# Kernel tuning notes

Measured on AMD Instinct MI355X. Metric: run time of the kernel, lower is better.

## Reference

```python
import jax, jax.numpy as jnp
import numpy as np

B, S, DIM = 2, 2048, 2048
H, KVH, D = 16, 8, 128
EPS = 1e-6
ROPE_BASE = 1000000.0
MAX_SEQ = 8192


def _build_rope(max_seq, dim, base):
    inv_freq = 1.0 / (base ** (np.arange(0, dim, 2, dtype=np.float64) / dim))
    t = np.arange(max_seq, dtype=np.float64)
    freqs = np.outer(t, inv_freq)  # [max_seq, dim//2]
    return (jnp.asarray(np.cos(freqs), jnp.float32),
            jnp.asarray(np.sin(freqs), jnp.float32))


def setup_inputs() -> dict:
    key = jax.random.key(0)
    ks = jax.random.split(key, 7)
    scale = 0.02
    cos_cache, sin_cache = _build_rope(MAX_SEQ, D, ROPE_BASE)
    return {
        "x": jax.random.normal(ks[0], (B, S, DIM), jnp.float32),
        "wq": jax.random.normal(ks[1], (DIM, H * D), jnp.float32) * scale,
        "wk": jax.random.normal(ks[2], (DIM, KVH * D), jnp.float32) * scale,
        "wv": jax.random.normal(ks[3], (DIM, KVH * D), jnp.float32) * scale,
        "wo": jax.random.normal(ks[4], (H * D, DIM), jnp.float32) * scale,
        "q_gamma": 1.0 + 0.01 * jax.random.normal(ks[5], (D,), jnp.float32),
        "k_gamma": 1.0 + 0.01 * jax.random.normal(ks[6], (D,), jnp.float32),
        "cos_cache": cos_cache,
        "sin_cache": sin_cache,
    }


def _rmsnorm(t, gamma):
    var = jnp.mean(t * t, axis=-1, keepdims=True)
    return t * jax.lax.rsqrt(var + EPS) * gamma


def _rotate_half(t):
    t1, t2 = jnp.split(t, 2, axis=-1)
    return jnp.concatenate((-t2, t1), axis=-1)


def _apply_rope(t, cos, sin):
    # t: [B, S, heads, D]; cos/sin: [S, D//2]
    cos_f = jnp.concatenate((cos, cos), axis=-1)[None, :, None, :]
    sin_f = jnp.concatenate((sin, sin), axis=-1)[None, :, None, :]
    return t * cos_f + _rotate_half(t) * sin_f


def reference(x, wq, wk, wv, wo, q_gamma, k_gamma, cos_cache, sin_cache):
    b, s, _ = x.shape
    q = (x @ wq).reshape(b, s, H, D)
    k = (x @ wk).reshape(b, s, KVH, D)
    v = (x @ wv).reshape(b, s, KVH, D)
    q = _rmsnorm(q, q_gamma)
    k = _rmsnorm(k, k_gamma)
    # prefill: kv_len == q_len == s, cache empty
    cos, sin = cos_cache[:s], sin_cache[:s]
    q = _apply_rope(q, cos, sin)
    k = _apply_rope(k, cos, sin)
    # -> [B, heads, S, D]
    q = q.transpose(0, 2, 1, 3)
    k = k.transpose(0, 2, 1, 3)
    v = v.transpose(0, 2, 1, 3)
    # GQA: repeat_interleave kv heads
    g = H // KVH
    k = jnp.repeat(k, g, axis=1)
    v = jnp.repeat(v, g, axis=1)
    scale = 1.0 / jnp.sqrt(jnp.asarray(D, x.dtype))
    scores = jnp.einsum("bhqd,bhkd->bhqk", q, k) * scale
    causal = jnp.tril(jnp.ones((s, s), bool))
    scores = jnp.where(causal, scores, jnp.finfo(scores.dtype).min)
    attn = jax.nn.softmax(scores, axis=-1)
    out = jnp.einsum("bhqk,bhkd->bhqd", attn, v)
    out = out.transpose(0, 2, 1, 3).reshape(b, s, H * D)
    return out @ wo
```

## Files before the change

### kernel.cpp

```cpp
#include <hip/hip_runtime.h>
#include <hip/hip_bf16.h>


typedef __attribute__((ext_vector_type(8))) short s16x8;
typedef __attribute__((ext_vector_type(4))) float f32x4;

typedef const __attribute__((address_space(1))) void* gas_t;
typedef __attribute__((address_space(3))) void* las_t;
#define GLL16(g, l) __builtin_amdgcn_global_load_lds((gas_t)(const void*)(g), (las_t)(void*)(l), 16, 0, 0)

static __device__ __forceinline__ unsigned short f2bf(float f) {
    union { float f; unsigned u; } v; v.f = f;
    unsigned r = v.u + 0x7FFF + ((v.u >> 16) & 1);
    return (unsigned short)(r >> 16);
}
static __device__ __forceinline__ float bf2f(unsigned short h) {
    union { unsigned u; float f; } v; v.u = ((unsigned)h) << 16;
    return v.f;
}
static __device__ __forceinline__ float exp2_fast(float x) {
    float r; asm("v_exp_f32 %0, %1" : "=v"(r) : "v"(x)); return r;
}

#define SCALE_L2E 0.12751744900929f

__global__ __launch_bounds__(256) void k_convert_x(const float* __restrict__ x,
                                                   unsigned short* __restrict__ xb, int n) {
    int i = (blockIdx.x * 256 + threadIdx.x) * 8;
    if (i >= n) return;
    float4 a = *(const float4*)(x + i);
    float4 b = *(const float4*)(x + i + 4);
    s16x8 o;
    o[0] = (short)f2bf(a.x); o[1] = (short)f2bf(a.y); o[2] = (short)f2bf(a.z); o[3] = (short)f2bf(a.w);
    o[4] = (short)f2bf(b.x); o[5] = (short)f2bf(b.y); o[6] = (short)f2bf(b.z); o[7] = (short)f2bf(b.w);
    *(s16x8*)(xb + i) = o;
}

__global__ __launch_bounds__(256) void k_transpose_w(const float* __restrict__ src,
                                                     unsigned short* __restrict__ dst,
                                                     int K, int N, int nbase, int dstld) {
    __shared__ float t[32][33];
    int k0 = blockIdx.x * 32, n0 = blockIdx.y * 32;
    int tx = threadIdx.x & 31, ty0 = threadIdx.x >> 5;
    for (int p = 0; p < 4; p++) {
        int ty = ty0 + p * 8;
        t[ty][tx] = src[(size_t)(k0 + ty) * N + n0 + tx];
    }
    __syncthreads();
    for (int p = 0; p < 4; p++) {
        int ty = ty0 + p * 8;
        dst[(size_t)(nbase + n0 + ty) * dstld + k0 + tx] = f2bf(t[tx][ty]);
    }
}

__global__ __launch_bounds__(256) void k_transpose_v(const unsigned short* __restrict__ V,
                                                     unsigned short* __restrict__ Vt) {
    __shared__ unsigned short t[32][33];
    int s0 = blockIdx.x * 32, d0 = blockIdx.y * 32;
    size_t base = (size_t)blockIdx.z * 2048 * 128;
    int tx = threadIdx.x & 31, ty0 = threadIdx.x >> 5;
    for (int p = 0; p < 4; p++) {
        int ty = ty0 + p * 8;
        t[ty][tx] = V[base + (size_t)(s0 + ty) * 128 + d0 + tx];
    }
    __syncthreads();
    for (int p = 0; p < 4; p++) {
        int ty = ty0 + p * 8;
        Vt[base + (size_t)(d0 + ty) * 2048 + s0 + tx] = t[tx][ty];
    }
}

template<int OUTF32>
__global__ __launch_bounds__(512, 2) void k_gemm256(const unsigned short* __restrict__ A,
                                                    const unsigned short* __restrict__ Bt,
                                                    void* __restrict__ Cout,
                                                    int M, int N, int K) {
    __shared__ unsigned short As[2][256 * 64];
    __shared__ unsigned short Bs[2][256 * 64];
    int tid = threadIdx.x, lane = tid & 63, wave = tid >> 6;
    int wm = wave >> 2, wn = wave & 3;
    int lr = lane & 15, lg = lane >> 4;
    int srow = wave * 8 + (lane >> 3);
    int scol = (((lane & 7) ^ (lane >> 3)) * 8);
    const unsigned short* Ag = A  + (size_t)(blockIdx.x * 256 + srow) * K + scol;
    const unsigned short* Bg = Bt + (size_t)(blockIdx.y * 256 + srow) * K + scol;
    int ldsoff = wave * 512;

    f32x4 acc[8][4] = {};
    int NK = K / 64;
    #pragma unroll
    for (int p = 0; p < 4; p++) {
        GLL16(Ag + (size_t)p * 64 * K, &As[0][p * 4096 + ldsoff]);
        GLL16(Bg + (size_t)p * 64 * K, &Bs[0][p * 4096 + ldsoff]);
    }
    for (int t = 0; t < NK; ++t) {
        int slot = t & 1, nslot = slot ^ 1;
        size_t kn = (size_t)(t + 1) * 64;
        bool more = (t + 1) < NK;
        if (more) {
            GLL16(Ag + kn, &As[nslot][ldsoff]);
            GLL16(Bg + kn, &Bs[nslot][ldsoff]);
            asm volatile("s_waitcnt vmcnt(2)" ::: "memory");
        } else {
            asm volatile("s_waitcnt vmcnt(0)" ::: "memory");
        }
        __builtin_amdgcn_s_barrier();
        asm volatile("" ::: "memory");
        s16x8 bf[4][2];
        #pragma unroll
        for (int n = 0; n < 4; n++)
            #pragma unroll
            for (int kk = 0; kk < 2; kk++)
                bf[n][kk] = *(const s16x8*)&Bs[slot][(wn * 64 + n * 16 + lr) * 64 +
                                                     ((kk * 32 + lg * 8) ^ ((lr & 7) << 3))];
        #pragma unroll
        for (int q = 0; q < 4; q++) {
            s16x8 af[2][2];
            #pragma unroll
            for (int mm = 0; mm < 2; mm++)
                #pragma unroll
                for (int kk = 0; kk < 2; kk++)
                    af[mm][kk] = *(const s16x8*)&As[slot][(wm * 128 + (q * 2 + mm) * 16 + lr) * 64 +
                                                          ((kk * 32 + lg * 8) ^ ((lr & 7) << 3))];
            if (more && q < 3) {
                GLL16(Ag + (size_t)(q + 1) * 64 * K + kn, &As[nslot][(q + 1) * 4096 + ldsoff]);
                GLL16(Bg + (size_t)(q + 1) * 64 * K + kn, &Bs[nslot][(q + 1) * 4096 + ldsoff]);
            }
            __builtin_amdgcn_s_barrier();
            __builtin_amdgcn_s_setprio(1);
            #pragma unroll
            for (int mm = 0; mm < 2; mm++)
                #pragma unroll
                for (int n = 0; n < 4; n++)
                    #pragma unroll
                    for (int kk = 0; kk < 2; kk++)
                        acc[q * 2 + mm][n] = __builtin_amdgcn_mfma_f32_16x16x32_bf16(
                            af[mm][kk], bf[n][kk], acc[q * 2 + mm][n], 0, 0, 0);
            __builtin_amdgcn_s_setprio(0);
            __builtin_amdgcn_s_barrier();
        }
    }
    int rbase = blockIdx.x * 256 + wm * 128;
    int cbase = blockIdx.y * 256 + wn * 64;
    #pragma unroll
    for (int am = 0; am < 8; am++)
        #pragma unroll
        for (int n = 0; n < 4; n++)
            #pragma unroll
            for (int r = 0; r < 4; r++) {
                int row = rbase + am * 16 + lg * 4 + r;
                int col = cbase + n * 16 + lr;
                float v = acc[am][n][r];
                if (OUTF32) ((float*)Cout)[(size_t)row * N + col] = v;
                else        ((unsigned short*)Cout)[(size_t)row * N + col] = f2bf(v);
            }
}

template<int OUTF32>
__global__ __launch_bounds__(256) void k_gemm_bt(const unsigned short* __restrict__ A,
                                                 const unsigned short* __restrict__ Bt,
                                                 void* __restrict__ Cout,
                                                 int M, int N, int K) {
    __shared__ unsigned short As[128 * 32];
    __shared__ unsigned short Bs[128 * 32];
    int tid = threadIdx.x;
    int lane = tid & 63;
    int wave = tid >> 6;
    int wm = wave >> 1, wn = wave & 1;
    int lr = lane & 15, lk = (lane >> 4) * 8;
    int srow = wave * 32 + (lane >> 2);
    int scol = (lane & 3) * 8;
    const unsigned short* Ag0 = A  + (size_t)(blockIdx.x * 128 + srow) * K + scol;
    const unsigned short* Ag1 = Ag0 + (size_t)16 * K;
    const unsigned short* Bg0 = Bt + (size_t)(blockIdx.y * 128 + srow) * K + scol;
    const unsigned short* Bg1 = Bg0 + (size_t)16 * K;
    unsigned short* Asw = &As[wave * 1024];
    unsigned short* Bsw = &Bs[wave * 1024];
    f32x4 acc[4][4] = {};
    for (int k0 = 0; k0 < K; k0 += 32) {
        __syncthreads();
        GLL16(Ag0 + k0, Asw);
        GLL16(Ag1 + k0, Asw + 512);
        GLL16(Bg0 + k0, Bsw);
        GLL16(Bg1 + k0, Bsw + 512);
        __syncthreads();
        s16x8 af[4], bfr[4];
        #pragma unroll
        for (int m = 0; m < 4; m++) af[m]  = *(const s16x8*)&As[(wm * 64 + m * 16 + lr) * 32 + lk];
        #pragma unroll
        for (int n = 0; n < 4; n++) bfr[n] = *(const s16x8*)&Bs[(wn * 64 + n * 16 + lr) * 32 + lk];
        #pragma unroll
        for (int m = 0; m < 4; m++)
            #pragma unroll
            for (int n = 0; n < 4; n++)
                acc[m][n] = __builtin_amdgcn_mfma_f32_16x16x32_bf16(af[m], bfr[n], acc[m][n], 0, 0, 0);
    }
    int rbase = blockIdx.x * 128 + wm * 64;
    int cbase = blockIdx.y * 128 + wn * 64;
    #pragma unroll
    for (int m = 0; m < 4; m++)
        #pragma unroll
        for (int n = 0; n < 4; n++)
            #pragma unroll
            for (int r = 0; r < 4; r++) {
                int row = rbase + m * 16 + (lane >> 4) * 4 + r;
                int col = cbase + n * 16 + lr;
                float v = acc[m][n][r];
                if (OUTF32) ((float*)Cout)[(size_t)row * N + col] = v;
                else        ((unsigned short*)Cout)[(size_t)row * N + col] = f2bf(v);
            }
}

__global__ __launch_bounds__(256) void k_rms_rope(const unsigned short* __restrict__ qkv,
                                                  const float* __restrict__ qg,
                                                  const float* __restrict__ kg,
                                                  const float* __restrict__ cosc,
                                                  const float* __restrict__ sinc,
                                                  unsigned short* __restrict__ Qt,
                                                  unsigned short* __restrict__ Kt,
                                                  unsigned short* __restrict__ Vt) {
    int r = blockIdx.x;
    int b = r >> 11;
    int s = r & 2047;
    int tid = threadIdx.x;
    int wave = tid >> 6, lane = tid & 63;
    int sl = lane >> 4;
    int li = lane & 15;
    int d0 = li * 8;
    const unsigned short* row = qkv + (size_t)r * 4096;
    #pragma unroll
    for (int p = 0; p < 2; p++) {
        int seg = p * 16 + wave * 4 + sl;
        s16x8 raw = *(const s16x8*)(row + seg * 128 + d0);
        if (seg >= 24) {
            *(s16x8*)(Vt + ((size_t)(b * 8 + (seg - 24)) * 2048 + s) * 128 + d0) = raw;
            continue;
        }
        float e[8];
        #pragma unroll
        for (int j = 0; j < 8; j++) e[j] = bf2f((unsigned short)raw[j]);
        float ssq = 0.f;
        #pragma unroll
        for (int j = 0; j < 8; j++) ssq += e[j] * e[j];
        ssq += __shfl_xor(ssq, 1, 64);
        ssq += __shfl_xor(ssq, 2, 64);
        ssq += __shfl_xor(ssq, 4, 64);
        ssq += __shfl_xor(ssq, 8, 64);
        float rn = rsqrtf(ssq * (1.0f / 128.0f) + 1e-6f);
        const float* g = (seg < 16) ? qg : kg;
        float gs = (seg < 16) ? SCALE_L2E : 1.0f;
        float4 g0 = *(const float4*)(g + d0);
        float4 g1 = *(const float4*)(g + d0 + 4);
        float t[8];
        t[0] = e[0] * rn * g0.x * gs; t[1] = e[1] * rn * g0.y * gs;
        t[2] = e[2] * rn * g0.z * gs; t[3] = e[3] * rn * g0.w * gs;
        t[4] = e[4] * rn * g1.x * gs; t[5] = e[5] * rn * g1.y * gs;
        t[6] = e[6] * rn * g1.z * gs; t[7] = e[7] * rn * g1.w * gs;
        float pr[8];
        #pragma unroll
        for (int j = 0; j < 8; j++) pr[j] = __shfl_xor(t[j], 8, 64);
        int didx = d0 & 63;
        float4 c0 = *(const float4*)(cosc + (size_t)s * 64 + didx);
        float4 c1 = *(const float4*)(cosc + (size_t)s * 64 + didx + 4);
        float4 sn0 = *(const float4*)(sinc + (size_t)s * 64 + didx);
        float4 sn1 = *(const float4*)(sinc + (size_t)s * 64 + didx + 4);
        float cv[8] = {c0.x, c0.y, c0.z, c0.w, c1.x, c1.y, c1.z, c1.w};
        float sv[8] = {sn0.x, sn0.y, sn0.z, sn0.w, sn1.x, sn1.y, sn1.z, sn1.w};
        float sgn = (li < 8) ? -1.0f : 1.0f;
        s16x8 o;
        #pragma unroll
        for (int j = 0; j < 8; j++)
            o[j] = (short)f2bf(t[j] * cv[j] + sgn * pr[j] * sv[j]);
        unsigned short* dst = (seg < 16)
            ? Qt + ((size_t)(b * 16 + seg) * 2048 + s) * 128 + d0
            : Kt + ((size_t)(b * 8 + (seg - 16)) * 2048 + s) * 128 + d0;
        *(s16x8*)dst = o;
    }
}

__global__ __launch_bounds__(512, 4) void k_attn(const unsigned short* __restrict__ Qt,
                                                 const unsigned short* __restrict__ Kt,
                                                 const unsigned short* __restrict__ Vtg,
                                                 unsigned short* __restrict__ attn) {
    __shared__ unsigned short Ks[64][136];
    __shared__ unsigned short Vs[128][72];
    __shared__ unsigned short Ps[8][16][72];
    int bid = blockIdx.x;
    int lo = bid & 255;
    int qb, bh;
    if (bid < 256) { qb = lo & 15;        bh = lo >> 4; }
    else           { qb = 15 - (lo & 15); bh = 16 + (lo >> 4); }
    int b = bh >> 4, h = bh & 15;
    int kvh = h >> 1;
    int tid = threadIdx.x;
    int lane = tid & 63, wave = tid >> 6;
    int lr = lane & 15, lg = lane >> 4;
    int q0 = qb * 128;
    const unsigned short* Qb1 = Qt + ((size_t)bh * 2048 + q0 + wave * 16) * 128;
    const unsigned short* Kbase = Kt + (size_t)(b * 8 + kvh) * 2048 * 128;
    const unsigned short* Vtb   = Vtg + (size_t)(b * 8 + kvh) * 128 * 2048;
    s16x8 aq[4];
    #pragma unroll
    for (int f = 0; f < 4; f++)
        aq[f] = *(const s16x8*)(Qb1 + (size_t)lr * 128 + f * 32 + lg * 8);
    f32x4 out[8] = {};
    float m_q = -1e30f, l_q = 0.f;
    int qglob = q0 + wave * 16 + lr;
    int qlo   = q0 + wave * 16;
    int qhi   = qlo + 15;
    int ntiles = 2 * qb + 2;
    int krow = tid >> 4, kcol = (tid & 15) * 8;
    int vrow = tid >> 3, vcol = (tid & 7) * 8;
    s16x8 kpre[2], vpre[2];
    #pragma unroll
    for (int p = 0; p < 2; p++) {
        kpre[p] = *(const s16x8*)(Kbase + (size_t)(krow + p * 32) * 128 + kcol);
        vpre[p] = *(const s16x8*)(Vtb + (size_t)(vrow + p * 64) * 2048 + vcol);
    }

    for (int t = 0; t < ntiles; t++) {
        int k0 = t * 64;
        __syncthreads();
        #pragma unroll
        for (int p = 0; p < 2; p++) {
            *(s16x8*)&Ks[krow + p * 32][kcol] = kpre[p];
            *(s16x8*)&Vs[vrow + p * 64][vcol] = vpre[p];
        }
        __syncthreads();
        if (t + 1 < ntiles) {
            int kn = k0 + 64;
            #pragma unroll
            for (int p = 0; p < 2; p++) {
                kpre[p] = *(const s16x8*)(Kbase + (size_t)(kn + krow + p * 32) * 128 + kcol);
                vpre[p] = *(const s16x8*)(Vtb + (size_t)(vrow + p * 64) * 2048 + kn + vcol);
            }
        }
        if (k0 <= qhi) {
            f32x4 st[4] = {};
            __builtin_amdgcn_s_setprio(1);
            #pragma unroll
            for (int sub = 0; sub < 4; sub++)
                #pragma unroll
                for (int f = 0; f < 4; f++) {
                    s16x8 bk = *(const s16x8*)&Ks[sub * 16 + lr][f * 32 + lg * 8];
                    st[sub] = __builtin_amdgcn_mfma_f32_16x16x32_bf16(bk, aq[f], st[sub], 0, 0, 0);
                }
            __builtin_amdgcn_s_setprio(0);
            float mx = -1e30f;
            if (k0 + 63 > qlo) {
                #pragma unroll
                for (int sub = 0; sub < 4; sub++)
                    #pragma unroll
                    for (int r = 0; r < 4; r++) {
                        int kv = k0 + sub * 16 + lg * 4 + r;
                        if (kv > qglob) st[sub][r] = -1e30f;
                        mx = fmaxf(mx, st[sub][r]);
                    }
            } else {
                #pragma unroll
                for (int sub = 0; sub < 4; sub++)
                    #pragma unroll
                    for (int r = 0; r < 4; r++) mx = fmaxf(mx, st[sub][r]);
            }
            mx = fmaxf(mx, __shfl_xor(mx, 16, 64));
            mx = fmaxf(mx, __shfl_xor(mx, 32, 64));
            bool defer = __all(mx <= m_q + 8.0f);
            float sf = 1.0f;
            if (!defer) {
                float mnew = fmaxf(m_q, mx);
                sf = exp2_fast(m_q - mnew);
                m_q = mnew;
            }
            float rs = 0.f;
            #pragma unroll
            for (int sub = 0; sub < 4; sub++)
                #pragma unroll
                for (int r = 0; r < 4; r++) {
                    float e = exp2_fast(st[sub][r] - m_q);
                    st[sub][r] = e;
                    rs += e;
                }
            rs += __shfl_xor(rs, 16, 64);
            rs += __shfl_xor(rs, 32, 64);
            l_q = defer ? (l_q + rs) : (l_q * sf + rs);
            #pragma unroll
            for (int sub = 0; sub < 4; sub++) {
                unsigned lop  = (unsigned)f2bf(st[sub][0]) | ((unsigned)f2bf(st[sub][1]) << 16);
                unsigned hip_ = (unsigned)f2bf(st[sub][2]) | ((unsigned)f2bf(st[sub][3]) << 16);
                uint2 w; w.x = lop; w.y = hip_;
                *(uint2*)&Ps[wave][lr][sub * 16 + lg * 4] = w;
            }
            if (!defer) {
                float sfr[4];
                #pragma unroll
                for (int r = 0; r < 4; r++) sfr[r] = __shfl(sf, lg * 4 + r, 64);
                #pragma unroll
                for (int blk = 0; blk < 8; blk++)
                    #pragma unroll
                    for (int r = 0; r < 4; r++) out[blk][r] *= sfr[r];
            }
            __builtin_amdgcn_s_setprio(1);
            #pragma unroll
            for (int ks = 0; ks < 2; ks++) {
                s16x8 ap = *(const s16x8*)&Ps[wave][lr][ks * 32 + lg * 8];
                #pragma unroll
                for (int blk = 0; blk < 8; blk++) {
                    s16x8 bv = *(const s16x8*)&Vs[blk * 16 + lr][ks * 32 + lg * 8];
                    out[blk] = __builtin_amdgcn_mfma_f32_16x16x32_bf16(ap, bv, out[blk], 0, 0, 0);
                }
            }
            __builtin_amdgcn_s_setprio(0);
        }
    }
    float linv = 1.0f / l_q;
    float inv[4];
    #pragma unroll
    for (int r = 0; r < 4; r++) inv[r] = __shfl(linv, lg * 4 + r, 64);
    #pragma unroll
    for (int blk = 0; blk < 8; blk++)
        #pragma unroll
        for (int r = 0; r < 4; r++) {
            int row = q0 + wave * 16 + lg * 4 + r;
            attn[((size_t)(b * 2048) + row) * 2048 + h * 128 + blk * 16 + lr] =
                f2bf(out[blk][r] * inv[r]);
        }
}

extern "C" void kernel_launch(void* const* d_in, const int* in_sizes, int n_in,
                              void* d_out, int out_size, void* d_ws, size_t ws_size,
                              hipStream_t stream) {
    const float* x    = (const float*)d_in[0];
    const float* wq   = (const float*)d_in[1];
    const float* wk   = (const float*)d_in[2];
    const float* wv   = (const float*)d_in[3];
    const float* wo   = (const float*)d_in[4];
    const float* qg   = (const float*)d_in[5];
    const float* kg   = (const float*)d_in[6];
    const float* cosc = (const float*)d_in[7];
    const float* sinc = (const float*)d_in[8];

    char* ws = (char*)d_ws;
    unsigned short* xb   = (unsigned short*)(ws);
    unsigned short* w1t  = (unsigned short*)(ws + 16777216);
    unsigned short* w2t  = (unsigned short*)(ws + 33554432);
    unsigned short* qkv  = (unsigned short*)(ws + 41943040);
    unsigned short* Qt   = (unsigned short*)(ws + 75497472);
    unsigned short* Kt   = (unsigned short*)(ws + 92274688);
    unsigned short* Vt   = (unsigned short*)(ws + 100663296);
    unsigned short* attn = (unsigned short*)(ws + 109051904);
    unsigned short* Vtg  = qkv;

    k_convert_x<<<4096, 256, 0, stream>>>(x, xb, 8388608);
    k_transpose_w<<<dim3(64, 64), 256, 0, stream>>>(wq, w1t, 2048, 2048, 0, 2048);
    k_transpose_w<<<dim3(64, 32), 256, 0, stream>>>(wk, w1t, 2048, 1024, 2048, 2048);
    k_transpose_w<<<dim3(64, 32), 256, 0, stream>>>(wv, w1t, 2048, 1024, 3072, 2048);
    k_transpose_w<<<dim3(64, 64), 256, 0, stream>>>(wo, w2t, 2048, 2048, 0, 2048);
    k_gemm256<0><<<dim3(16, 16), 512, 0, stream>>>(xb, w1t, qkv, 4096, 4096, 2048);
    k_rms_rope<<<4096, 256, 0, stream>>>(qkv, qg, kg, cosc, sinc, Qt, Kt, Vt);
    k_transpose_v<<<dim3(64, 4, 16), 256, 0, stream>>>(Vt, Vtg);
    k_attn<<<512, 512, 0, stream>>>(Qt, Kt, Vtg, attn);
    k_gemm_bt<1><<<dim3(32, 16), 256, 0, stream>>>(attn, w2t, d_out, 4096, 2048, 2048);
}
```

Baseline: 239.2 us.

## Restructure 256x256 GEMM main loop into k-half sub-tiles with finer prefetch

Splits each 64-wide K tile of the LDS staging into two 32-wide halves per matrix, using a new XOR swizzle for the 32-column layout. The main loop runs in four phases, each issuing one quarter of the next tile's global-to-LDS loads and then running a 16-MFMA block. The intent is to overlap loads with compute more evenly and cut LDS bank conflicts and register pressure (fewer live fragments). The cost is more barriers per iteration and tricky vmcnt accounting that could be wrong.

```diff
diff --git a/kernel.cpp b/kernel.cpp
--- a/kernel.cpp
+++ b/kernel.cpp
@@ -75,71 +75,109 @@
                                                     const unsigned short* __restrict__ Bt,
                                                     void* __restrict__ Cout,
                                                     int M, int N, int K) {
-    __shared__ unsigned short As[2][256 * 64];
-    __shared__ unsigned short Bs[2][256 * 64];
+    __shared__ unsigned short Ls[2][2][2][8192];
     int tid = threadIdx.x, lane = tid & 63, wave = tid >> 6;
     int wm = wave >> 2, wn = wave & 3;
     int lr = lane & 15, lg = lane >> 4;
-    int srow = wave * 8 + (lane >> 3);
-    int scol = (((lane & 7) ^ (lane >> 3)) * 8);
-    const unsigned short* Ag = A  + (size_t)(blockIdx.x * 256 + srow) * K + scol;
-    const unsigned short* Bg = Bt + (size_t)(blockIdx.y * 256 + srow) * K + scol;
-    int ldsoff = wave * 512;
+    int swrow = wave * 16 + (lane >> 2);
+    int ssw   = ((lane >> 2) & 3) ^ lg;
+    int scol  = ((lane & 3) ^ ssw) * 8;
+    const unsigned short* Ab = A  + (size_t)(blockIdx.x * 256) * K;
+    const unsigned short* Bb = Bt + (size_t)(blockIdx.y * 256) * K;
+    int cgr = (lg ^ (lr & 3) ^ ((lr >> 2) & 3)) * 8;
 
     f32x4 acc[8][4] = {};
     int NK = K / 64;
-    #pragma unroll
-    for (int p = 0; p < 4; p++) {
-        GLL16(Ag + (size_t)p * 64 * K, &As[0][p * 4096 + ldsoff]);
-        GLL16(Bg + (size_t)p * 64 * K, &Bs[0][p * 4096 + ldsoff]);
-    }
+
+    auto issue = [&](int slot, int mat, int kk, int k0) {
+        const unsigned short* base = mat ? Bb : Ab;
+        unsigned short* dst = &Ls[slot][mat][kk][wave * 512];
+        GLL16(base + (size_t)swrow * K + k0 + kk * 32 + scol, dst);
+        GLL16(base + (size_t)(swrow + 128) * K + k0 + kk * 32 + scol, dst + 4096);
+    };
+
+    issue(0, 0, 0, 0);
+    issue(0, 1, 0, 0);
+    issue(0, 0, 1, 0);
+    issue(0, 1, 1, 0);
+
     for (int t = 0; t < NK; ++t) {
         int slot = t & 1, nslot = slot ^ 1;
-        size_t kn = (size_t)(t + 1) * 64;
+        int kn = (t + 1) * 64;
         bool more = (t + 1) < NK;
-        if (more) {
-            GLL16(Ag + kn, &As[nslot][ldsoff]);
-            GLL16(Bg + kn, &Bs[nslot][ldsoff]);
-            asm volatile("s_waitcnt vmcnt(2)" ::: "memory");
-        } else {
-            asm volatile("s_waitcnt vmcnt(0)" ::: "memory");
-        }
-        __builtin_amdgcn_s_barrier();
-        asm volatile("" ::: "memory");
-        s16x8 bf[4][2];
-        #pragma unroll
-        for (int n = 0; n < 4; n++)
-            #pragma unroll
-            for (int kk = 0; kk < 2; kk++)
-                bf[n][kk] = *(const s16x8*)&Bs[slot][(wn * 64 + n * 16 + lr) * 64 +
-                                                     ((kk * 32 + lg * 8) ^ ((lr & 7) << 3))];
-        #pragma unroll
-        for (int q = 0; q < 4; q++) {
-            s16x8 af[2][2];
-            #pragma unroll
-            for (int mm = 0; mm < 2; mm++)
-                #pragma unroll
-                for (int kk = 0; kk < 2; kk++)
-                    af[mm][kk] = *(const s16x8*)&As[slot][(wm * 128 + (q * 2 + mm) * 16 + lr) * 64 +
-                                                          ((kk * 32 + lg * 8) ^ ((lr & 7) << 3))];
-            if (more && q < 3) {
-                GLL16(Ag + (size_t)(q + 1) * 64 * K + kn, &As[nslot][(q + 1) * 4096 + ldsoff]);
-                GLL16(Bg + (size_t)(q + 1) * 64 * K + kn, &Bs[nslot][(q + 1) * 4096 + ldsoff]);
-            }
-            __builtin_amdgcn_s_barrier();
-            __builtin_amdgcn_s_setprio(1);
-            #pragma unroll
-            for (int mm = 0; mm < 2; mm++)
-                #pragma unroll
-                for (int n = 0; n < 4; n++)
-                    #pragma unroll
-                    for (int kk = 0; kk < 2; kk++)
-                        acc[q * 2 + mm][n] = __builtin_amdgcn_mfma_f32_16x16x32_bf16(
-                            af[mm][kk], bf[n][kk], acc[q * 2 + mm][n], 0, 0, 0);
-            __builtin_amdgcn_s_setprio(0);
-            __builtin_amdgcn_s_barrier();
-        }
-    }
+        const unsigned short* As0 = Ls[slot][0][0];
+        const unsigned short* Bs0 = Ls[slot][1][0];
+        const unsigned short* As1 = Ls[slot][0][1];
+        const unsigned short* Bs1 = Ls[slot][1][1];
+        s16x8 af[4], bfr[4];
+
+        if (more) { issue(nslot, 0, 0, kn); asm volatile("s_waitcnt vmcnt(6)" ::: "memory"); }
+        else      {                         asm volatile("s_waitcnt vmcnt(4)" ::: "memory"); }
+        __builtin_amdgcn_s_barrier();
+        asm volatile("" ::: "memory");
+        #pragma unroll
+        for (int m = 0; m < 4; m++) af[m]  = *(const s16x8*)&As0[(wm * 128 + m * 16 + lr) * 32 + cgr];
+        #pragma unroll
+        for (int n = 0; n < 4; n++) bfr[n] = *(const s16x8*)&Bs0[(wn * 64 + n * 16 + lr) * 32 + cgr];
+        __builtin_amdgcn_s_setprio(1);
+        #pragma unroll
+        for (int m = 0; m < 4; m++)
+            #pragma unroll
+            for (int n = 0; n < 4; n++)
+                acc[m][n] = __builtin_amdgcn_mfma_f32_16x16x32_bf16(af[m], bfr[n], acc[m][n], 0, 0, 0);
+        __builtin_amdgcn_s_setprio(0);
+        asm volatile("" ::: "memory");
+        __builtin_amdgcn_s_barrier();
+
+        if (more) issue(nslot, 1, 0, kn);
+        __builtin_amdgcn_s_barrier();
+        asm volatile("" ::: "memory");
+        #pragma unroll
+        for (int m = 0; m < 4; m++) af[m] = *(const s16x8*)&As0[(wm * 128 + (m + 4) * 16 + lr) * 32 + cgr];
+        __builtin_amdgcn_s_setprio(1);
+        #pragma unroll
+        for (int m = 0; m < 4; m++)
+            #pragma unroll
+            for (int n = 0; n < 4; n++)
+                acc[m + 4][n] = __builtin_amdgcn_mfma_f32_16x16x32_bf16(af[m], bfr[n], acc[m + 4][n], 0, 0, 0);
+        __builtin_amdgcn_s_setprio(0);
+        asm volatile("" ::: "memory");
+        __builtin_amdgcn_s_barrier();
+
+        if (more) { issue(nslot, 0, 1, kn); asm volatile("s_waitcnt vmcnt(6)" ::: "memory"); }
+        else      {                         asm volatile("s_waitcnt vmcnt(0)" ::: "memory"); }
+        __builtin_amdgcn_s_barrier();
+        asm volatile("" ::: "memory");
+        #pragma unroll
+        for (int m = 0; m < 4; m++) af[m]  = *(const s16x8*)&As1[(wm * 128 + m * 16 + lr) * 32 + cgr];
+        #pragma unroll
+        for (int n = 0; n < 4; n++) bfr[n] = *(const s16x8*)&Bs1[(wn * 64 + n * 16 + lr) * 32 + cgr];
+        __builtin_amdgcn_s_setprio(1);
+        #pragma unroll
+        for (int m = 0; m < 4; m++)
+            #pragma unroll
+            for (int n = 0; n < 4; n++)
+                acc[m][n] = __builtin_amdgcn_mfma_f32_16x16x32_bf16(af[m], bfr[n], acc[m][n], 0, 0, 0);
+        __builtin_amdgcn_s_setprio(0);
+        asm volatile("" ::: "memory");
+        __builtin_amdgcn_s_barrier();
+
+        if (more) issue(nslot, 1, 1, kn);
+        __builtin_amdgcn_s_barrier();
+        asm volatile("" ::: "memory");
+        #pragma unroll
+        for (int m = 0; m < 4; m++) af[m] = *(const s16x8*)&As1[(wm * 128 + (m + 4) * 16 + lr) * 32 + cgr];
+        __builtin_amdgcn_s_setprio(1);
+        #pragma unroll
+        for (int m = 0; m < 4; m++)
+            #pragma unroll
+            for (int n = 0; n < 4; n++)
+                acc[m + 4][n] = __builtin_amdgcn_mfma_f32_16x16x32_bf16(af[m], bfr[n], acc[m + 4][n], 0, 0, 0);
+        __builtin_amdgcn_s_setprio(0);
+        asm volatile("" ::: "memory");
+        __builtin_amdgcn_s_barrier();
+    }
+
     int rbase = blockIdx.x * 256 + wm * 128;
     int cbase = blockIdx.y * 256 + wn * 64;
     #pragma unroll
```

Result: no change. 236.6 us (-1.1%).
